# Kernel tuning notes

Measured on AMD Instinct MI355X. Metric: run time of the kernel, lower is better.

## Reference

```python
import jax, jax.numpy as jnp
import numpy as np

E_DIM = 64
N_EMBED = 1024
N_TOKENS = 262144


def setup_inputs() -> dict:
    key = jax.random.key(0)
    k1, k2 = jax.random.split(key)
    inp = jax.random.normal(k1, (N_TOKENS, E_DIM), dtype=jnp.float32)
    # codebook init mirrors torch uniform_(-1/n_embed, 1/n_embed)
    embed = jax.random.uniform(k2, (E_DIM, N_EMBED), dtype=jnp.float32,
                               minval=-1.0 / N_EMBED, maxval=1.0 / N_EMBED)
    return {"input": inp, "embed": embed}


def reference(input, embed):
    e_dim, n_embed = embed.shape
    flatten = input.reshape(-1, e_dim)  # [N, e_dim]
    dist = (jnp.sum(flatten * flatten, axis=1, keepdims=True)
            - 2.0 * flatten @ embed
            + jnp.sum(embed * embed, axis=0, keepdims=True))
    embed_idxs = jnp.argmin(dist, axis=1)  # matches (-dist).max(1) indices
    embed_idxs = embed_idxs.reshape(input.shape[:-1])
    quantize = jnp.take(embed.T, embed_idxs, axis=0)  # gather codes -> [..., e_dim]
    # straight-through estimator
    quantize_input_grad = input + jax.lax.stop_gradient(quantize - input)
    return (quantize, input, quantize_input_grad, embed_idxs, embed)
```

## Files before the change

### kernel.cpp

```cpp
#include <hip/hip_runtime.h>
#include <hip/hip_bf16.h>
#include <math.h>

#define E_DIM    64
#define N_EMBED  1024
#define N_TOKENS 262144
#define FQCAP    32768

typedef __attribute__((ext_vector_type(8)))  short bf16x8;
typedef __attribute__((ext_vector_type(16))) float f32x16;


__device__ __forceinline__ short f2bf_bits(float f) {
    __hip_bfloat16 h = __float2bfloat16(f);
    return *reinterpret_cast<short*>(&h);
}
__device__ __forceinline__ float bfbits2f(short s) {
    unsigned int u = ((unsigned int)(unsigned short)s) << 16;
    return __uint_as_float(u);
}

__device__ __forceinline__ float exact_d(const float* __restrict__ xrow,
                                         const float* __restrict__ emb,
                                         const float* __restrict__ csum,
                                         float a, int j) {
#pragma clang fp contract(off)
    float b = 0.f;
#pragma unroll
    for (int k = 0; k < E_DIM; ++k) b = fmaf(xrow[k], emb[k * N_EMBED + j], b);
    return (a - 2.0f * b) + csum[j];
}

__device__ __forceinline__ float a_np_of(const float* x) {
#pragma clang fp contract(off)
    float s[16];
#pragma unroll
    for (int i = 0; i < 16; ++i)
        s[i] = (x[i] * x[i] + x[i + 16] * x[i + 16]) +
               (x[i + 32] * x[i + 32] + x[i + 48] * x[i + 48]);
    float hh[8];
#pragma unroll
    for (int i = 0; i < 8; ++i) hh[i] = s[i] + s[i + 8];
    float uu[4];
#pragma unroll
    for (int i = 0; i < 4; ++i) uu[i] = hh[i] + hh[i + 4];
    return (uu[0] + uu[2]) + (uu[1] + uu[3]);
}

__device__ __forceinline__ bool lexless(float av, int ai, float bv, int bi) {
    return (av < bv) || (av == bv && ai < bi);
}

__global__ __launch_bounds__(256) void vq_prep(const float* __restrict__ emb,
                                               short* __restrict__ eTc,
                                               float* __restrict__ out_e,
                                               float* __restrict__ embT,
                                               float* __restrict__ c_out,
                                               unsigned int* __restrict__ qcnt) {
    const int b = blockIdx.x;
    if (b < 256) {
        const int t = b * 256 + threadIdx.x;
        const int k = t >> 10, n = t & 1023;
        float e = emb[t];
        float m2 = -2.0f * e;
        short hb = f2bf_bits(m2);
        short lb = f2bf_bits(m2 - bfbits2f(hb));
        const int chunk = n >> 7, code = n & 127, slot = k >> 3, jj = k & 7;
        const int base = chunk * 16384 + (slot * 128 + code) * 8 + jj;
        eTc[base]        = hb;
        eTc[base + 8192] = lb;
        out_e[t] = e;
        embT[n * E_DIM + k] = e;
    } else {
#pragma clang fp contract(off)
        if (b == 256 && threadIdx.x == 0) qcnt[0] = 0;
        const int j = (b - 256) * 256 + threadIdx.x;
        float e = emb[j];
        float s = e * e;
        for (int k = 1; k < E_DIM; ++k) {
            float ek = emb[k * N_EMBED + j];
            float pk = ek * ek;
            s = s + pk;
        }
        c_out[j] = s;
    }
}

__device__ __forceinline__ void tile_epilogue(
    const f32x16& acc, int codebase_global, int h,
    float& v1, float& v2, float& v3, int& i1, int& i2) {
#pragma unroll
    for (int r = 0; r < 16; ++r) {
        const int row = (r & 3) + 8 * (r >> 2) + 4 * h;
        const float d = acc[r];
        const int idx = codebase_global + row;
        if (d < v3) {
            if (d < v1)      { v3 = v2; v2 = v1; i2 = i1; v1 = d; i1 = idx; }
            else if (d < v2) { v3 = v2; v2 = d;  i2 = idx; }
            else             { v3 = d; }
        }
    }
}

__global__ __launch_bounds__(256, 4) void vq_screen_kernel(
    const float* __restrict__ in, const float* __restrict__ emb,
    const float* __restrict__ csum, const short* __restrict__ eTc,
    float* __restrict__ out_idx, float* __restrict__ out_in,
    unsigned int* __restrict__ qcnt, unsigned int* __restrict__ fullQ)
{
    __shared__ uint4 lds_e[2048];

    const int t = threadIdx.x;
    const int wave = t >> 6, l = t & 63, col = l & 31, h = l >> 5;
    const int tok = blockIdx.x * 128 + wave * 32 + col;
    const float* xrow = in + (size_t)tok * E_DIM;
    const size_t obase = (size_t)tok * E_DIM;

    float xv[4][8];
#pragma unroll
    for (int s = 0; s < 4; ++s) {
        float4 u0 = *reinterpret_cast<const float4*>(xrow + s * 16 + h * 8);
        float4 u1 = *reinterpret_cast<const float4*>(xrow + s * 16 + h * 8 + 4);
        xv[s][0] = u0.x; xv[s][1] = u0.y; xv[s][2] = u0.z; xv[s][3] = u0.w;
        xv[s][4] = u1.x; xv[s][5] = u1.y; xv[s][6] = u1.z; xv[s][7] = u1.w;
        *reinterpret_cast<float4*>(out_in + obase + s * 16 + h * 8)     = u0;
        *reinterpret_cast<float4*>(out_in + obase + s * 16 + h * 8 + 4) = u1;
    }
    bf16x8 bhi[4], blo[4];
    float sax_h = 0.f;
#pragma unroll
    for (int s = 0; s < 4; ++s) {
#pragma unroll
        for (int j = 0; j < 8; ++j) {
            float x = xv[s][j];
            sax_h += fabsf(x);
            short hb = f2bf_bits(x);
            bhi[s][j] = hb;
            blo[s][j] = f2bf_bits(x - bfbits2f(hb));
        }
    }
    const float sax = sax_h + __shfl_xor(sax_h, 32, 64);

    float a_np;
    {
#pragma clang fp contract(off)
        float sv[8];
#pragma unroll
        for (int j = 0; j < 8; ++j) {
            float p0 = xv[0][j] * xv[0][j];
            float p1 = xv[1][j] * xv[1][j];
            float p2 = xv[2][j] * xv[2][j];
            float p3 = xv[3][j] * xv[3][j];
            sv[j] = (p0 + p1) + (p2 + p3);
        }
        float hh[8];
#pragma unroll
        for (int j = 0; j < 8; ++j) hh[j] = sv[j] + __shfl_xor(sv[j], 32, 64);
        float u0 = hh[0] + hh[4], u1 = hh[1] + hh[5];
        float u2 = hh[2] + hh[6], u3 = hh[3] + hh[7];
        a_np = (u0 + u2) + (u1 + u3);
    }

    float v1 = 3.4e38f, v2 = 3.4e38f, v3 = 3.4e38f;
    int i1 = 0, i2 = 0;

    for (int cc = 0; cc < 8; ++cc) {
        __syncthreads();
        {
            const uint4* gsrc = reinterpret_cast<const uint4*>(eTc) + cc * 2048;
#pragma unroll
            for (int j = 0; j < 8; ++j) lds_e[j * 256 + t] = gsrc[j * 256 + t];
        }
        __syncthreads();

        const int cb = cc << 7;
#pragma unroll
        for (int tp = 0; tp < 2; ++tp) {
            const int c0 = tp * 64 + col;
            const int cbase = cb + tp * 64 + 4 * h;
            const float4 cA0 = *reinterpret_cast<const float4*>(&csum[cbase + 0]);
            const float4 cA1 = *reinterpret_cast<const float4*>(&csum[cbase + 8]);
            const float4 cA2 = *reinterpret_cast<const float4*>(&csum[cbase + 16]);
            const float4 cA3 = *reinterpret_cast<const float4*>(&csum[cbase + 24]);
            const float4 cB0 = *reinterpret_cast<const float4*>(&csum[cbase + 32]);
            const float4 cB1 = *reinterpret_cast<const float4*>(&csum[cbase + 40]);
            const float4 cB2 = *reinterpret_cast<const float4*>(&csum[cbase + 48]);
            const float4 cB3 = *reinterpret_cast<const float4*>(&csum[cbase + 56]);
            f32x16 accA, accB;
            accA[0]=cA0.x;  accA[1]=cA0.y;  accA[2]=cA0.z;  accA[3]=cA0.w;
            accA[4]=cA1.x;  accA[5]=cA1.y;  accA[6]=cA1.z;  accA[7]=cA1.w;
            accA[8]=cA2.x;  accA[9]=cA2.y;  accA[10]=cA2.z; accA[11]=cA2.w;
            accA[12]=cA3.x; accA[13]=cA3.y; accA[14]=cA3.z; accA[15]=cA3.w;
            accB[0]=cB0.x;  accB[1]=cB0.y;  accB[2]=cB0.z;  accB[3]=cB0.w;
            accB[4]=cB1.x;  accB[5]=cB1.y;  accB[6]=cB1.z;  accB[7]=cB1.w;
            accB[8]=cB2.x;  accB[9]=cB2.y;  accB[10]=cB2.z; accB[11]=cB2.w;
            accB[12]=cB3.x; accB[13]=cB3.y; accB[14]=cB3.z; accB[15]=cB3.w;
#pragma unroll
            for (int s = 0; s < 4; ++s) {
                const int slot = 2 * s + h;
                bf16x8 ahA = *reinterpret_cast<const bf16x8*>(&lds_e[slot * 128 + c0]);
                bf16x8 alA = *reinterpret_cast<const bf16x8*>(&lds_e[1024 + slot * 128 + c0]);
                bf16x8 ahB = *reinterpret_cast<const bf16x8*>(&lds_e[slot * 128 + c0 + 32]);
                bf16x8 alB = *reinterpret_cast<const bf16x8*>(&lds_e[1024 + slot * 128 + c0 + 32]);
                accA = __builtin_amdgcn_mfma_f32_32x32x16_bf16(ahA, bhi[s], accA, 0, 0, 0);
                accB = __builtin_amdgcn_mfma_f32_32x32x16_bf16(ahB, bhi[s], accB, 0, 0, 0);
                accA = __builtin_amdgcn_mfma_f32_32x32x16_bf16(ahA, blo[s], accA, 0, 0, 0);
                accB = __builtin_amdgcn_mfma_f32_32x32x16_bf16(ahB, blo[s], accB, 0, 0, 0);
                accA = __builtin_amdgcn_mfma_f32_32x32x16_bf16(alA, bhi[s], accA, 0, 0, 0);
                accB = __builtin_amdgcn_mfma_f32_32x32x16_bf16(alB, bhi[s], accB, 0, 0, 0);
            }
            tile_epilogue(accA, cb + tp * 64,      h, v1, v2, v3, i1, i2);
            tile_epilogue(accB, cb + tp * 64 + 32, h, v1, v2, v3, i1, i2);
        }
    }

    const float w1 = __shfl_xor(v1, 32, 64), w2 = __shfl_xor(v2, 32, 64), w3 = __shfl_xor(v3, 32, 64);
    const int   j1 = __shfl_xor(i1, 32, 64), j2 = __shfl_xor(i2, 32, 64);
    const bool bfirst = lexless(w1, j1, v1, i1);
    const float r1v = bfirst ? w1 : v1;  const int r1i = bfirst ? j1 : i1;
    const float cav = bfirst ? v1 : v2;  const int cai = bfirst ? i1 : i2;
    const float cbv = bfirst ? w2 : w1;  const int cbi = bfirst ? j2 : j1;
    const bool bsec = lexless(cbv, cbi, cav, cai);
    const float r2v = bsec ? cbv : cav;  const int r2i = bsec ? cbi : cai;
    const float r3v = bsec ? fminf(cav, bfirst ? w3 : w2)
                           : fminf(cbv, bfirst ? v2 : v3);

    if (l < 32) {
        const float thr = 8e-5f + 4e-7f * sax;
        const bool sane = (a_np < 150.f) && (sax < 128.f) && (fabsf(r1v) < 0.5f);
        int fin = r1i;
        if (sane && (r2v - r1v > thr)) {
        } else if (sane && (r3v - r1v > thr)) {
            const float d1 = exact_d(xrow, emb, csum, a_np, r1i);
            const float d2 = exact_d(xrow, emb, csum, a_np, r2i);
            if (d2 < d1 || (d2 == d1 && r2i < r1i)) fin = r2i;
        } else {
            const unsigned int qi = atomicAdd(qcnt, 1u);
            if (qi < FQCAP) fullQ[qi] = (unsigned int)tok;
        }
        out_idx[tok] = (float)fin;
    }
}

__global__ __launch_bounds__(256) void vq_full_kernel(
    const float* __restrict__ in, const float* __restrict__ emb,
    const float* __restrict__ csum, const unsigned int* __restrict__ qcnt,
    const unsigned int* __restrict__ fullQ, float* __restrict__ out_idx) {
#pragma clang fp contract(off)
    unsigned int nq = *qcnt;
    if (nq > FQCAP) nq = FQCAP;
    const int l = threadIdx.x & 63;
    for (unsigned int w = blockIdx.x * 4 + (threadIdx.x >> 6); w < nq; w += 1024) {
        const int tok = (int)fullQ[w];
        const float* xrow = in + (size_t)tok * E_DIM;
        float x[E_DIM];
#pragma unroll
        for (int j4 = 0; j4 < 16; ++j4) {
            const float4 u = *reinterpret_cast<const float4*>(xrow + j4 * 4);
            x[j4 * 4 + 0] = u.x; x[j4 * 4 + 1] = u.y;
            x[j4 * 4 + 2] = u.z; x[j4 * 4 + 3] = u.w;
        }
        const float a = a_np_of(x);
        const int c0 = l * 16;
        float b[16];
#pragma unroll
        for (int q = 0; q < 16; ++q) b[q] = 0.f;
        for (int k = 0; k < E_DIM; ++k) {
            const float xk = x[k];
            const float* er = emb + k * N_EMBED + c0;
#pragma unroll
            for (int q = 0; q < 16; ++q) b[q] = fmaf(xk, er[q], b[q]);
        }
        float bd = 3.4e38f; int bi = 1 << 30;
#pragma unroll
        for (int q = 0; q < 16; ++q) {
            const float d = (a - 2.0f * b[q]) + csum[c0 + q];
            if (d < bd) { bd = d; bi = c0 + q; }
        }
        for (int m = 1; m < 64; m <<= 1) {
            const float od = __shfl_xor(bd, m, 64);
            const int oi = __shfl_xor(bi, m, 64);
            if (od < bd || (od == bd && oi < bi)) { bd = od; bi = oi; }
        }
        if (l == 0) out_idx[tok] = (float)bi;
    }
}

__global__ __launch_bounds__(256) void vq_gather_kernel(
    const float* __restrict__ in, const float* __restrict__ embT,
    const float* __restrict__ idxf,
    float* __restrict__ out_q, float* __restrict__ out_g) {
#pragma clang fp contract(off)
    const size_t j = (size_t)blockIdx.x * 256 + threadIdx.x;
    const int m  = (int)(j >> 4);
    const int k0 = ((int)j & 15) * 4;
    const int idx = (int)idxf[m];

    const float4 x = reinterpret_cast<const float4*>(in)[j];
    const float4 q = *reinterpret_cast<const float4*>(&embT[(size_t)idx * E_DIM + k0]);

    float4 g;
    g.x = x.x + (q.x - x.x);
    g.y = x.y + (q.y - x.y);
    g.z = x.z + (q.z - x.z);
    g.w = x.w + (q.w - x.w);

    reinterpret_cast<float4*>(out_q)[j] = q;
    reinterpret_cast<float4*>(out_g)[j] = g;
}

extern "C" void kernel_launch(void* const* d_in, const int* in_sizes, int n_in,
                              void* d_out, int out_size, void* d_ws, size_t ws_size,
                              hipStream_t stream) {
    const float* in  = (const float*)d_in[0];
    const float* emb = (const float*)d_in[1];

    float* out     = (float*)d_out;
    float* out_q   = out;
    float* out_in  = out + (size_t)N_TOKENS * E_DIM;
    float* out_g   = out + 2ull * N_TOKENS * E_DIM;
    float* out_idx = out + 3ull * N_TOKENS * E_DIM;
    float* out_e   = out_idx + N_TOKENS;

    unsigned char* ws = (unsigned char*)d_ws;
    float*          c_ws  = (float*)(ws);
    short*          eTc   = (short*)(ws + 4096);
    float*          embT  = (float*)(ws + 4096 + 262144);
    unsigned int*   qcnt  = (unsigned int*)(ws + 4096 + 262144 + 262144);
    unsigned int*   fullQ = (unsigned int*)(ws + 4096 + 262144 + 262144 + 256);

    vq_prep<<<260, 256, 0, stream>>>(emb, eTc, out_e, embT, c_ws, qcnt);

    vq_screen_kernel<<<N_TOKENS / 128, 256, 0, stream>>>(
        in, emb, c_ws, eTc, out_idx, out_in, qcnt, fullQ);

    vq_full_kernel<<<256, 256, 0, stream>>>(in, emb, c_ws, qcnt, fullQ, out_idx);

    const int gather_blocks = (N_TOKENS * E_DIM / 4) / 256;
    vq_gather_kernel<<<gather_blocks, 256, 0, stream>>>(in, embT, out_idx,
                                                        out_q, out_g);
}
```

Before: 267.7 us.

## Store codebook in MFMA fragment order and read it directly from global

```diff
diff --git a/kernel.cpp b/kernel.cpp
--- a/kernel.cpp
+++ b/kernel.cpp
@@ -65,10 +65,16 @@
         float m2 = -2.0f * e;
         short hb = f2bf_bits(m2);
         short lb = f2bf_bits(m2 - bfbits2f(hb));
-        const int chunk = n >> 7, code = n & 127, slot = k >> 3, jj = k & 7;
-        const int base = chunk * 16384 + (slot * 128 + code) * 8 + jj;
-        eTc[base]        = hb;
-        eTc[base + 8192] = lb;
+        const int chunk = n >> 7;
+        const int tp = (n & 127) >> 6;
+        const int c_local = n & 63;
+        const int whichAB = c_local >> 5, col = c_local & 31;
+        const int slot = k >> 3, s = slot >> 1, h = slot & 1, j = k & 7;
+        const int lane = h * 32 + col;
+        const int fragHi = (tp * 4 + s) * 4 + whichAB * 2;
+        const int base = chunk * 16384 + lane * 8 + j;
+        eTc[base + fragHi * 512]       = hb;
+        eTc[base + (fragHi + 1) * 512] = lb;
         out_e[t] = e;
         embT[n * E_DIM + k] = e;
     } else {
@@ -108,8 +114,6 @@
     float* __restrict__ out_idx, float* __restrict__ out_in,
     unsigned int* __restrict__ qcnt, unsigned int* __restrict__ fullQ)
 {
-    __shared__ uint4 lds_e[2048];
-
     const int t = threadIdx.x;
     const int wave = t >> 6, l = t & 63, col = l & 31, h = l >> 5;
     const int tok = blockIdx.x * 128 + wave * 32 + col;
@@ -164,19 +168,12 @@
     float v1 = 3.4e38f, v2 = 3.4e38f, v3 = 3.4e38f;
     int i1 = 0, i2 = 0;
 
+    const short* gch = eTc + l * 8;
+
     for (int cc = 0; cc < 8; ++cc) {
-        __syncthreads();
-        {
-            const uint4* gsrc = reinterpret_cast<const uint4*>(eTc) + cc * 2048;
-#pragma unroll
-            for (int j = 0; j < 8; ++j) lds_e[j * 256 + t] = gsrc[j * 256 + t];
-        }
-        __syncthreads();
-
         const int cb = cc << 7;
 #pragma unroll
         for (int tp = 0; tp < 2; ++tp) {
-            const int c0 = tp * 64 + col;
             const int cbase = cb + tp * 64 + 4 * h;
             const float4 cA0 = *reinterpret_cast<const float4*>(&csum[cbase + 0]);
             const float4 cA1 = *reinterpret_cast<const float4*>(&csum[cbase + 8]);
@@ -197,11 +194,11 @@
             accB[12]=cB3.x; accB[13]=cB3.y; accB[14]=cB3.z; accB[15]=cB3.w;
 #pragma unroll
             for (int s = 0; s < 4; ++s) {
-                const int slot = 2 * s + h;
-                bf16x8 ahA = *reinterpret_cast<const bf16x8*>(&lds_e[slot * 128 + c0]);
-                bf16x8 alA = *reinterpret_cast<const bf16x8*>(&lds_e[1024 + slot * 128 + c0]);
-                bf16x8 ahB = *reinterpret_cast<const bf16x8*>(&lds_e[slot * 128 + c0 + 32]);
-                bf16x8 alB = *reinterpret_cast<const bf16x8*>(&lds_e[1024 + slot * 128 + c0 + 32]);
+                const int fb = cc * 16384 + ((tp * 4 + s) * 4) * 512;
+                const bf16x8 ahA = *reinterpret_cast<const bf16x8*>(gch + fb + 0 * 512);
+                const bf16x8 alA = *reinterpret_cast<const bf16x8*>(gch + fb + 1 * 512);
+                const bf16x8 ahB = *reinterpret_cast<const bf16x8*>(gch + fb + 2 * 512);
+                const bf16x8 alB = *reinterpret_cast<const bf16x8*>(gch + fb + 3 * 512);
                 accA = __builtin_amdgcn_mfma_f32_32x32x16_bf16(ahA, bhi[s], accA, 0, 0, 0);
                 accB = __builtin_amdgcn_mfma_f32_32x32x16_bf16(ahB, bhi[s], accB, 0, 0, 0);
                 accA = __builtin_amdgcn_mfma_f32_32x32x16_bf16(ahA, blo[s], accA, 0, 0, 0);
```

Result: slower. 286.0 us (+6.9%).
